# Kernel tuning notes

Measured on AMD Instinct MI355X. Metric: run time of the kernel, lower is better.

The kernel has to match this reference:

```python
import jax, jax.numpy as jnp
import numpy as np

ALPHA = 0.2  # LeakyReLU negative slope
NEG_INF = -9e15


def _gat_layer(Wh, adj, a, concat):
    """One GraphAttentionLayer given pre-projected Wh [B,N,F].
    Algebraic split of the concat attention: e[b,i,j] = lrelu(Wh[i]@a1 + Wh[j]@a2),
    identical math to matmul(cat(Wh_i, Wh_j), a)."""
    F_ = Wh.shape[-1]
    f1 = Wh @ a[:F_, 0]   # [B,N]
    f2 = Wh @ a[F_:, 0]   # [B,N]
    e = jax.nn.leaky_relu(f1[:, :, None] + f2[:, None, :], negative_slope=ALPHA)  # [B,N,N]
    e = jnp.where(adj > 0, e, NEG_INF)
    att = jax.nn.softmax(e, axis=-1)            # dropout omitted (eval mode)
    h_prime = jnp.einsum('bij,bjf->bif', att, Wh)
    return jax.nn.elu(h_prime) if concat else h_prime


def setup_inputs() -> dict:
    key = jax.random.key(0)
    ks = jax.random.split(key, 9)
    B, N, Fin, H, nH, Fout = 4, 2048, 512, 128, 4, 256
    x = jax.random.normal(ks[0], (B, N, Fin), dtype=jnp.float32)
    adj = jax.random.randint(ks[1], (B, N, N), 0, 2, dtype=jnp.int32)
    mask = jnp.ones((B, N), dtype=jnp.float32)
    s = 0.05
    W_heads = jax.random.normal(ks[2], (nH, Fin, H), dtype=jnp.float32) * s
    a_heads = jax.random.normal(ks[3], (nH, 2 * H, 1), dtype=jnp.float32) * s
    W_out = jax.random.normal(ks[4], (nH * H, Fout), dtype=jnp.float32) * s
    a_out = jax.random.normal(ks[5], (2 * Fout, 1), dtype=jnp.float32) * s
    W_pool = jax.random.normal(ks[6], (Fout, Fout), dtype=jnp.float32) * s
    b_pool = jax.random.normal(ks[7], (Fout,), dtype=jnp.float32) * s
    return {"x": x, "adj": adj, "mask": mask, "W_heads": W_heads, "a_heads": a_heads,
            "W_out": W_out, "a_out": a_out, "W_pool": W_pool, "b_pool": b_pool}


def reference(x, adj, mask, W_heads, a_heads, W_out, a_out, W_pool, b_pool):
    # multi-head GAT layer, heads concatenated (dropout = identity in eval)
    heads = [_gat_layer(x @ W_heads[h], adj, a_heads[h], concat=True)
             for h in range(W_heads.shape[0])]
    xcat = jnp.concatenate(heads, axis=-1)                 # [B,N,nH*H]
    x_out = _gat_layer(xcat @ W_out, adj, a_out, concat=False)  # [B,N,Fout]
    x_out = x_out * mask[:, :, None]
    pooled = x_out.sum(axis=1) / (mask.sum(axis=1, keepdims=True) + 1e-10)
    graph_embedding = jax.nn.relu(pooled @ W_pool + b_pool)
    return graph_embedding, x_out
```

## Files before the change

kernel.cpp:

```cpp
#include <hip/hip_runtime.h>

typedef unsigned short u16;
typedef __attribute__((ext_vector_type(8))) short s8v;
typedef __attribute__((ext_vector_type(8))) unsigned short us8;
typedef __attribute__((ext_vector_type(4))) float f4v;

#define L2E 1.4426950408889634f

typedef __attribute__((address_space(1))) void gvoid_t;
typedef __attribute__((address_space(3))) void lvoid_t;

__device__ __forceinline__ u16 f2bf(float f) {
  unsigned u = __builtin_bit_cast(unsigned, f);
  return (u16)((u + 0x7FFFu + ((u >> 16) & 1u)) >> 16);
}
__device__ __forceinline__ float bf2f(u16 h) {
  return __builtin_bit_cast(float, ((unsigned)h) << 16);
}
__device__ __forceinline__ f4v mfma16(s8v a, s8v b, f4v c) {
  return __builtin_amdgcn_mfma_f32_16x16x32_bf16(a, b, c, 0, 0, 0);
}
__device__ __forceinline__ float exp2fast(float x) {
#if __has_builtin(__builtin_amdgcn_exp2f)
  return __builtin_amdgcn_exp2f(x);
#else
  return exp2f(x);
#endif
}
__device__ __forceinline__ void stage16(const u16* g, u16* lds_arr, int slot) {
#if __has_builtin(__builtin_amdgcn_global_load_lds)
  __builtin_amdgcn_global_load_lds((gvoid_t*)(g),
      (lvoid_t*)(lds_arr + (size_t)(slot & ~63) * 8), 16, 0, 0);
#else
  *(us8*)(lds_arr + (size_t)slot * 8) = *(const us8*)g;
#endif
}

__global__ __launch_bounds__(256) void prep_x(const float* __restrict__ x,
                                              u16* __restrict__ xb) {
  int i = (blockIdx.x * 256 + threadIdx.x) * 8;
  float4 v0 = *(const float4*)(x + i);
  float4 v1 = *(const float4*)(x + i + 4);
  us8 o;
  o[0] = f2bf(v0.x); o[1] = f2bf(v0.y); o[2] = f2bf(v0.z); o[3] = f2bf(v0.w);
  o[4] = f2bf(v1.x); o[5] = f2bf(v1.y); o[6] = f2bf(v1.z); o[7] = f2bf(v1.w);
  *(us8*)(xb + i) = o;
}

__global__ __launch_bounds__(256) void prep_wall(const float* __restrict__ W,
                                                 u16* __restrict__ Wt) {
  int idx = blockIdx.x * 256 + threadIdx.x;
  int h = idx >> 16, k = (idx >> 7) & 511, f = idx & 127;
  Wt[(size_t)(h * 128 + f) * 512 + k] = f2bf(W[idx]);
}
__global__ __launch_bounds__(256) void prep_wout(const float* __restrict__ W,
                                                 u16* __restrict__ Wt) {
  int idx = blockIdx.x * 256 + threadIdx.x;
  int k = idx >> 8, c = idx & 255;
  Wt[(size_t)c * 512 + k] = f2bf(W[idx]);
}
__global__ __launch_bounds__(256) void prep_adj(const int* __restrict__ adj,
                                                unsigned* __restrict__ adjw) {
  int chunk = blockIdx.x * 4 + (threadIdx.x >> 6);
  int l = threadIdx.x & 63;
  int v = adj[(size_t)chunk * 64 + l];
  unsigned long long m = __ballot(v != 0);
  if (l == 0) {
    ((uint2*)adjw)[chunk] = make_uint2((unsigned)m, (unsigned)(m >> 32));
  }
}

__global__ __launch_bounds__(256) void gemm_bf16(const u16* __restrict__ A,
                                                 const u16* __restrict__ Bt,
                                                 u16* __restrict__ Ct, int CO) {
  const int K = 512, N = 2048;
  int m0 = blockIdx.x * 128;
  int n0 = blockIdx.y * 128;
  int t = threadIdx.x;
  int w = t >> 6, l = t & 63, lr = l & 15, lq = l >> 4;
  int wr = w >> 1, wc = w & 1;
  __shared__ u16 As[2][128 * 32];
  __shared__ u16 Bs[2][128 * 32];
  f4v zero4 = {0.f, 0.f, 0.f, 0.f};
  f4v acc[4][4];
#pragma unroll
  for (int i = 0; i < 4; ++i)
#pragma unroll
    for (int j = 0; j < 4; ++j) acc[i][j] = zero4;

  auto stage = [&](int buf, int kt) {
    int k0 = kt * 32;
    int row = t >> 2, ch = t & 3;
    stage16(A + (size_t)(m0 + row) * K + k0 + ch * 8, As[buf], t);
    stage16(Bt + (size_t)(n0 + row) * K + k0 + ch * 8, Bs[buf], t);
    int s2 = t + 256;
    row = s2 >> 2; ch = s2 & 3;
    stage16(A + (size_t)(m0 + row) * K + k0 + ch * 8, As[buf], s2);
    stage16(Bt + (size_t)(n0 + row) * K + k0 + ch * 8, Bs[buf], s2);
  };
  stage(0, 0);
  for (int kt = 0; kt < 16; ++kt) {
    __syncthreads();
    if (kt < 15) stage((kt + 1) & 1, kt + 1);
    const u16* as = As[kt & 1];
    const u16* bs = Bs[kt & 1];
    s8v af[4], bfr[4];
#pragma unroll
    for (int rf = 0; rf < 4; ++rf)
      af[rf] = *(const s8v*)&as[(wr * 64 + rf * 16 + lr) * 32 + lq * 8];
#pragma unroll
    for (int nf = 0; nf < 4; ++nf)
      bfr[nf] = *(const s8v*)&bs[(wc * 64 + nf * 16 + lr) * 32 + lq * 8];
#pragma unroll
    for (int rf = 0; rf < 4; ++rf)
#pragma unroll
      for (int nf = 0; nf < 4; ++nf)
        acc[rf][nf] = mfma16(af[rf], bfr[nf], acc[rf][nf]);
  }
  int bidx = m0 >> 11;
  int nr0 = m0 & 2047;
#pragma unroll
  for (int rf = 0; rf < 4; ++rf) {
#pragma unroll
    for (int nf = 0; nf < 4; ++nf) {
      int col = n0 + wc * 64 + nf * 16 + lr;
      int nr = nr0 + wr * 64 + rf * 16 + lq * 4;
      f4v a = acc[rf][nf];
      ushort4 v = make_ushort4(f2bf(a[0]), f2bf(a[1]), f2bf(a[2]), f2bf(a[3]));
      *(ushort4*)&Ct[((size_t)bidx * CO + col) * N + nr] = v;
    }
  }
}

__global__ __launch_bounds__(256) void fkern(const u16* __restrict__ Wht,
                                             const float* __restrict__ a,
                                             float* __restrict__ f1L,
                                             float* __restrict__ f2L, int COLS,
                                             int F) {
  const int N = 2048;
  int h = blockIdx.z, b = blockIdx.y;
  int nl = threadIdx.x & 63, fc = threadIdx.x >> 6;
  int n = blockIdx.x * 64 + nl;
  int F4 = F >> 2;
  const u16* colp = Wht + ((size_t)(b * COLS + h * F + fc * F4)) * N + n;
  const float* ah = a + h * 2 * F + fc * F4;
  float a1 = 0.f, a2 = 0.f;
  for (int c = 0; c < F4; ++c) {
    float v = bf2f(colp[(size_t)c * N]);
    a1 = fmaf(v, ah[c], a1);
    a2 = fmaf(v, ah[F + c], a2);
  }
  __shared__ float r1[4][64], r2[4][64];
  r1[fc][nl] = a1;
  r2[fc][nl] = a2;
  __syncthreads();
  if (fc == 0) {
    float s1 = r1[0][nl] + r1[1][nl] + r1[2][nl] + r1[3][nl];
    float s2 = r2[0][nl] + r2[1][nl] + r2[2][nl] + r2[3][nl];
    f1L[(size_t)(h * 4 + b) * N + n] = s1 * L2E;
    f2L[(size_t)(h * 4 + b) * N + n] = s2 * L2E;
  }
}

__global__ __launch_bounds__(256) void fmax_kern(const float* __restrict__ f2L,
                                                 float* __restrict__ f2m) {
  int row = blockIdx.x;
  const float* p = f2L + (size_t)row * 2048;
  int t = threadIdx.x;
  float v = -__builtin_inff();
  for (int k = 0; k < 8; ++k) v = fmaxf(v, p[t + k * 256]);
#pragma unroll
  for (int d = 1; d < 64; d <<= 1) v = fmaxf(v, __shfl_xor(v, d));
  __shared__ float wm[4];
  if ((t & 63) == 0) wm[t >> 6] = v;
  __syncthreads();
  if (t == 0) f2m[row] = fmaxf(fmaxf(wm[0], wm[1]), fmaxf(wm[2], wm[3]));
}

template <int CT, bool ELU>
__global__ __launch_bounds__(256, 2) void attn_kernel(
    const u16* __restrict__ Wht, const float* __restrict__ f1L,
    const float* __restrict__ f2L, const float* __restrict__ f2max,
    const unsigned* __restrict__ adjw, const float* __restrict__ mask,
    void* __restrict__ outp) {
  const int N = 2048;
  constexpr int NCH = CT / 128;
  constexpr int ROWS = 64;
  constexpr int NT = 2048 / ROWS;
  constexpr int FHD = (CT == 512) ? 1 : 0;
  int kb = blockIdx.x;
  int x = kb & 7, g = kb >> 3;
  int p = x + 8 * (g / NT);
  int it = g % NT;
  int b = p / NCH, ch = p % NCH;
  int i0 = it * ROWS, col0 = ch * 128;
  int fh = FHD ? ch : 0;
  int t = threadIdx.x;
  int w = t >> 6, l = t & 63, lr = l & 15, lq = l >> 4;

  __shared__ u16 Vs[2][128 * 64];
  __shared__ unsigned adjs[ROWS * 65];
  __shared__ float f2s[2048];

  const float* f1p = f1L + (size_t)(fh * 4 + b) * N + i0;
  const float* f2p = f2L + (size_t)(fh * 4 + b) * N;
  float f2m = f2max[fh * 4 + b];
  float f1v = f1p[w * 16 + lr];
  float su = f1v + f2m;
  float M = fmaxf(su, 0.2f * su);
  float c1 = f1v - M;
  float c2 = 0.2f * f1v - M;
  const u16* vbase = Wht + (size_t)(b * CT + col0) * 2048;

  for (int i = t; i < ROWS * 64; i += 256) {
    int row = i >> 6, wd = i & 63;
    adjs[row * 65 + wd] = adjw[(size_t)(b * N + i0 + row) * 64 + wd];
  }
  for (int i = t; i < 2048; i += 256) f2s[i] = f2p[i];

  auto stage = [&](int buf, int kt) {
    int k0 = kt * 64;
#pragma unroll
    for (int j2 = 0; j2 < 4; ++j2) {
      int s = j2 * 256 + t;
      int c = s >> 3, q = s & 7;
      stage16(vbase + (size_t)c * 2048 + k0 + (q ^ (c & 7)) * 8, Vs[buf], s);
    }
  };
  stage(0, 0);

  f4v zero4 = {0.f, 0.f, 0.f, 0.f};
  f4v acc[8];
#pragma unroll
  for (int j = 0; j < 8; ++j) acc[j] = zero4;
  float s_ = 0.f;

  for (int kt = 0; kt < 32; ++kt) {
    __syncthreads();
    if (kt < 31) stage((kt + 1) & 1, kt + 1);
    const u16* vs = Vs[kt & 1];
#pragma unroll
    for (int kk = 0; kk < 2; ++kk) {
      int jt = kt * 2 + kk;
      s8v vf[8];
#pragma unroll
      for (int nf = 0; nf < 8; ++nf) {
        int chn = (kk * 4 + lq) ^ (lr & 7);
        vf[nf] = *(const s8v*)&vs[(nf * 16 + lr) * 64 + chn * 8];
      }
      float4 fa = *(const float4*)&f2s[jt * 32 + lq * 8];
      float4 fb = *(const float4*)&f2s[jt * 32 + lq * 8 + 4];
      float f2c[8] = {fa.x, fa.y, fa.z, fa.w, fb.x, fb.y, fb.z, fb.w};
      unsigned aw = adjs[(w * 16 + lr) * 65 + jt];
      union { s8v v; unsigned u[4]; } pk;
#pragma unroll
      for (int ep = 0; ep < 4; ++ep) {
        float t1 = c1 + f2c[2 * ep];
        float t2 = fmaf(0.2f, f2c[2 * ep], c2);
        float p0 = exp2fast(fmaxf(t1, t2));
        p0 = ((aw >> (lq * 8 + 2 * ep)) & 1u) ? p0 : 0.f;
        s_ += p0;
        float t3 = c1 + f2c[2 * ep + 1];
        float t4 = fmaf(0.2f, f2c[2 * ep + 1], c2);
        float p1 = exp2fast(fmaxf(t3, t4));
        p1 = ((aw >> (lq * 8 + 2 * ep + 1)) & 1u) ? p1 : 0.f;
        s_ += p1;
        asm("v_cvt_pk_bf16_f32 %0, %1, %2"
            : "=v"(pk.u[ep]) : "v"(p0), "v"(p1));
      }
      s8v pa = pk.v;
#pragma unroll
      for (int nf = 0; nf < 8; ++nf)
        acc[nf] = mfma16(pa, vf[nf], acc[nf]);
    }
  }
  s_ += __shfl_xor(s_, 16);
  s_ += __shfl_xor(s_, 32);
  float inv = 1.f / fmaxf(s_, 1e-30f);
  f4v i4;
#pragma unroll
  for (int r = 0; r < 4; ++r) i4[r] = __shfl(inv, lq * 4 + r);
  int rowb = i0 + w * 16 + lq * 4;
#pragma unroll
  for (int nf = 0; nf < 8; ++nf) {
    int col = col0 + nf * 16 + lr;
#pragma unroll
    for (int r = 0; r < 4; ++r) {
      float v = acc[nf][r] * i4[r];
      size_t ob = (size_t)(b * N + rowb + r) * CT + col;
      if constexpr (ELU) {
        v = v > 0.f ? v : exp2fast(v * L2E) - 1.f;
        ((u16*)outp)[ob] = f2bf(v);
      } else {
        ((float*)outp)[ob] = v * mask[b * N + rowb + r];
      }
    }
  }
}

__global__ __launch_bounds__(256) void pool1(const float* __restrict__ xout,
                                             const float* __restrict__ mask,
                                             float* __restrict__ pool,
                                             float* __restrict__ den) {
  int b = blockIdx.x >> 6, s = blockIdx.x & 63;
  int c = threadIdx.x;
  int n0 = s * 32;
  float acc = 0.f;
  for (int r = 0; r < 32; ++r)
    acc += xout[((size_t)(b * 2048 + n0 + r)) * 256 + c];
  atomicAdd(&pool[b * 256 + c], acc);
  if (c == 0) {
    float ms = 0.f;
    for (int r = 0; r < 32; ++r) ms += mask[b * 2048 + n0 + r];
    atomicAdd(&den[b], ms);
  }
}
__global__ __launch_bounds__(256) void pool2(const float* __restrict__ pool,
                                             const float* __restrict__ den,
                                             const float* __restrict__ Wp,
                                             const float* __restrict__ bp,
                                             float* __restrict__ out) {
  int b = blockIdx.x, f = threadIdx.x;
  __shared__ float pv[256];
  float inv = 1.f / (den[b] + 1e-10f);
  pv[f] = pool[b * 256 + f] * inv;
  __syncthreads();
  float acc = bp[f];
  for (int c = 0; c < 256; ++c) acc = fmaf(pv[c], Wp[c * 256 + f], acc);
  out[b * 256 + f] = fmaxf(acc, 0.f);
}

extern "C" void kernel_launch(void* const* d_in, const int* in_sizes, int n_in,
                              void* d_out, int out_size, void* d_ws,
                              size_t ws_size, hipStream_t stream) {
  (void)in_sizes; (void)n_in; (void)out_size; (void)ws_size;
  const float* x = (const float*)d_in[0];
  const int* adj = (const int*)d_in[1];
  const float* mask = (const float*)d_in[2];
  const float* Whds = (const float*)d_in[3];
  const float* ahds = (const float*)d_in[4];
  const float* Wout = (const float*)d_in[5];
  const float* aout = (const float*)d_in[6];
  const float* Wpool = (const float*)d_in[7];
  const float* bpool = (const float*)d_in[8];
  float* out = (float*)d_out;

  char* ws = (char*)d_ws;
  size_t off = 0;
  auto take = [&](size_t n) {
    char* p = ws + off;
    off += (n + 255) & ~(size_t)255;
    return p;
  };
  u16* xb = (u16*)take(8192ull * 512 * 2);
  u16* Wta = (u16*)take(512ull * 512 * 2);
  u16* Wto = (u16*)take(256ull * 512 * 2);
  unsigned* adjw = (unsigned*)take(4ull * 2048 * 64 * 4);
  u16* Wht = (u16*)take(4ull * 512 * 2048 * 2);
  float* f1a = (float*)take(4ull * 4 * 2048 * 4);
  float* f2a = (float*)take(4ull * 4 * 2048 * 4);
  u16* xcat = (u16*)take(8192ull * 512 * 2);
  u16* Wh2t = (u16*)take(4ull * 256 * 2048 * 2);
  float* f1b = (float*)take(4ull * 2048 * 4);
  float* f2b = (float*)take(4ull * 2048 * 4);
  float* f2ma = (float*)take(16 * 4);
  float* f2mb = (float*)take(4 * 4);
  float* pool = (float*)take(1024 * 4);
  float* den = (float*)take(256);

  prep_x<<<2048, 256, 0, stream>>>(x, xb);
  prep_wall<<<1024, 256, 0, stream>>>(Whds, Wta);
  prep_wout<<<512, 256, 0, stream>>>(Wout, Wto);
  prep_adj<<<65536, 256, 0, stream>>>(adj, adjw);
  gemm_bf16<<<dim3(64, 4), 256, 0, stream>>>(xb, Wta, Wht, 512);
  fkern<<<dim3(32, 4, 4), 256, 0, stream>>>(Wht, ahds, f1a, f2a, 512, 128);
  fmax_kern<<<16, 256, 0, stream>>>(f2a, f2ma);
  attn_kernel<512, true><<<512, 256, 0, stream>>>(Wht, f1a, f2a, f2ma,
                                                  adjw, nullptr, xcat);
  gemm_bf16<<<dim3(64, 2), 256, 0, stream>>>(xcat, Wto, Wh2t, 256);
  fkern<<<dim3(32, 4, 1), 256, 0, stream>>>(Wh2t, aout, f1b, f2b, 256, 256);
  fmax_kern<<<4, 256, 0, stream>>>(f2b, f2mb);
  attn_kernel<256, false><<<256, 256, 0, stream>>>(Wh2t, f1b, f2b, f2mb,
                                                   adjw, mask, out + 1024);
  hipMemsetAsync(pool, 0, 4096 + 256, stream);
  pool1<<<256, 256, 0, stream>>>(out + 1024, mask, pool, den);
  pool2<<<4, 256, 0, stream>>>(pool, den, Wpool, bpool, out);
}
```

Baseline: 180.5 us.

## Swizzle GEMM LDS tiles, compute softmax sums via MFMA, split second attention by rows/cols

Applies an XOR swizzle to the GEMM's shared-memory A/B tiles to cut LDS bank conflicts on fragment reads. In the attention kernel, the per-row softmax denominator is now computed with an extra MFMA against a ones vector instead of scalar adds plus shuffles. The attention kernel is also templated on a warp-row count, so the second (256-column) layer uses 32-row tiles with two column-warps and launches 512 blocks instead of 256, raising parallelism. The cost is one extra MFMA per step and more redundant exp work per output column in the second layer.

```diff
diff --git a/kernel.cpp b/kernel.cpp
--- a/kernel.cpp
+++ b/kernel.cpp
@@ -91,14 +91,17 @@
   auto stage = [&](int buf, int kt) {
     int k0 = kt * 32;
     int row = t >> 2, ch = t & 3;
-    stage16(A + (size_t)(m0 + row) * K + k0 + ch * 8, As[buf], t);
-    stage16(Bt + (size_t)(n0 + row) * K + k0 + ch * 8, Bs[buf], t);
+    int q = (ch ^ ((row >> 1) & 3)) * 8;
+    stage16(A + (size_t)(m0 + row) * K + k0 + q, As[buf], t);
+    stage16(Bt + (size_t)(n0 + row) * K + k0 + q, Bs[buf], t);
     int s2 = t + 256;
     row = s2 >> 2; ch = s2 & 3;
-    stage16(A + (size_t)(m0 + row) * K + k0 + ch * 8, As[buf], s2);
-    stage16(Bt + (size_t)(n0 + row) * K + k0 + ch * 8, Bs[buf], s2);
+    q = (ch ^ ((row >> 1) & 3)) * 8;
+    stage16(A + (size_t)(m0 + row) * K + k0 + q, As[buf], s2);
+    stage16(Bt + (size_t)(n0 + row) * K + k0 + q, Bs[buf], s2);
   };
   stage(0, 0);
+  int swz = (lq ^ ((lr >> 1) & 3)) * 8;
   for (int kt = 0; kt < 16; ++kt) {
     __syncthreads();
     if (kt < 15) stage((kt + 1) & 1, kt + 1);
@@ -107,10 +110,10 @@
     s8v af[4], bfr[4];
 #pragma unroll
     for (int rf = 0; rf < 4; ++rf)
-      af[rf] = *(const s8v*)&as[(wr * 64 + rf * 16 + lr) * 32 + lq * 8];
+      af[rf] = *(const s8v*)&as[(wr * 64 + rf * 16 + lr) * 32 + swz];
 #pragma unroll
     for (int nf = 0; nf < 4; ++nf)
-      bfr[nf] = *(const s8v*)&bs[(wc * 64 + nf * 16 + lr) * 32 + lq * 8];
+      bfr[nf] = *(const s8v*)&bs[(wc * 64 + nf * 16 + lr) * 32 + swz];
 #pragma unroll
     for (int rf = 0; rf < 4; ++rf)
 #pragma unroll
@@ -177,15 +180,17 @@
   if (t == 0) f2m[row] = fmaxf(fmaxf(wm[0], wm[1]), fmaxf(wm[2], wm[3]));
 }
 
-template <int CT, bool ELU>
+template <int CT, int WR, bool ELU>
 __global__ __launch_bounds__(256, 2) void attn_kernel(
     const u16* __restrict__ Wht, const float* __restrict__ f1L,
     const float* __restrict__ f2L, const float* __restrict__ f2max,
     const unsigned* __restrict__ adjw, const float* __restrict__ mask,
     void* __restrict__ outp) {
   const int N = 2048;
+  constexpr int WC = 4 / WR;
+  constexpr int NF = 8 / WC;
   constexpr int NCH = CT / 128;
-  constexpr int ROWS = 64;
+  constexpr int ROWS = WR * 16;
   constexpr int NT = 2048 / ROWS;
   constexpr int FHD = (CT == 512) ? 1 : 0;
   int kb = blockIdx.x;
@@ -197,6 +202,7 @@
   int fh = FHD ? ch : 0;
   int t = threadIdx.x;
   int w = t >> 6, l = t & 63, lr = l & 15, lq = l >> 4;
+  int wc = w & (WC - 1), wrs = w / WC;
 
   __shared__ u16 Vs[2][128 * 64];
   __shared__ unsigned adjs[ROWS * 65];
@@ -205,7 +211,7 @@
   const float* f1p = f1L + (size_t)(fh * 4 + b) * N + i0;
   const float* f2p = f2L + (size_t)(fh * 4 + b) * N;
   float f2m = f2max[fh * 4 + b];
-  float f1v = f1p[w * 16 + lr];
+  float f1v = f1p[wrs * 16 + lr];
   float su = f1v + f2m;
   float M = fmaxf(su, 0.2f * su);
   float c1 = f1v - M;
@@ -230,10 +236,12 @@
   stage(0, 0);
 
   f4v zero4 = {0.f, 0.f, 0.f, 0.f};
-  f4v acc[8];
-#pragma unroll
-  for (int j = 0; j < 8; ++j) acc[j] = zero4;
-  float s_ = 0.f;
+  f4v acc[NF], accs = zero4;
+#pragma unroll
+  for (int j = 0; j < NF; ++j) acc[j] = zero4;
+  s8v ones;
+#pragma unroll
+  for (int i = 0; i < 8; ++i) ones[i] = (short)0x3F80;
 
   for (int kt = 0; kt < 32; ++kt) {
     __syncthreads();
@@ -242,16 +250,17 @@
 #pragma unroll
     for (int kk = 0; kk < 2; ++kk) {
       int jt = kt * 2 + kk;
-      s8v vf[8];
-#pragma unroll
-      for (int nf = 0; nf < 8; ++nf) {
+      s8v vf[NF];
+#pragma unroll
+      for (int nf = 0; nf < NF; ++nf) {
+        int c = wc * 64 + nf * 16 + lr;
         int chn = (kk * 4 + lq) ^ (lr & 7);
-        vf[nf] = *(const s8v*)&vs[(nf * 16 + lr) * 64 + chn * 8];
+        vf[nf] = *(const s8v*)&vs[c * 64 + chn * 8];
       }
       float4 fa = *(const float4*)&f2s[jt * 32 + lq * 8];
       float4 fb = *(const float4*)&f2s[jt * 32 + lq * 8 + 4];
       float f2c[8] = {fa.x, fa.y, fa.z, fa.w, fb.x, fb.y, fb.z, fb.w};
-      unsigned aw = adjs[(w * 16 + lr) * 65 + jt];
+      unsigned aw = adjs[(wrs * 16 + lr) * 65 + jt];
       union { s8v v; unsigned u[4]; } pk;
 #pragma unroll
       for (int ep = 0; ep < 4; ++ep) {
@@ -259,31 +268,27 @@
         float t2 = fmaf(0.2f, f2c[2 * ep], c2);
         float p0 = exp2fast(fmaxf(t1, t2));
         p0 = ((aw >> (lq * 8 + 2 * ep)) & 1u) ? p0 : 0.f;
-        s_ += p0;
         float t3 = c1 + f2c[2 * ep + 1];
         float t4 = fmaf(0.2f, f2c[2 * ep + 1], c2);
         float p1 = exp2fast(fmaxf(t3, t4));
         p1 = ((aw >> (lq * 8 + 2 * ep + 1)) & 1u) ? p1 : 0.f;
-        s_ += p1;
         asm("v_cvt_pk_bf16_f32 %0, %1, %2"
             : "=v"(pk.u[ep]) : "v"(p0), "v"(p1));
       }
       s8v pa = pk.v;
-#pragma unroll
-      for (int nf = 0; nf < 8; ++nf)
+      accs = mfma16(pa, ones, accs);
+#pragma unroll
+      for (int nf = 0; nf < NF; ++nf)
         acc[nf] = mfma16(pa, vf[nf], acc[nf]);
     }
   }
-  s_ += __shfl_xor(s_, 16);
-  s_ += __shfl_xor(s_, 32);
-  float inv = 1.f / fmaxf(s_, 1e-30f);
   f4v i4;
 #pragma unroll
-  for (int r = 0; r < 4; ++r) i4[r] = __shfl(inv, lq * 4 + r);
-  int rowb = i0 + w * 16 + lq * 4;
-#pragma unroll
-  for (int nf = 0; nf < 8; ++nf) {
-    int col = col0 + nf * 16 + lr;
+  for (int r = 0; r < 4; ++r) i4[r] = 1.f / fmaxf(accs[r], 1e-30f);
+  int rowb = i0 + wrs * 16 + lq * 4;
+#pragma unroll
+  for (int nf = 0; nf < NF; ++nf) {
+    int col = col0 + wc * 64 + nf * 16 + lr;
 #pragma unroll
     for (int r = 0; r < 4; ++r) {
       float v = acc[nf][r] * i4[r];
@@ -375,13 +380,13 @@
   gemm_bf16<<<dim3(64, 4), 256, 0, stream>>>(xb, Wta, Wht, 512);
   fkern<<<dim3(32, 4, 4), 256, 0, stream>>>(Wht, ahds, f1a, f2a, 512, 128);
   fmax_kern<<<16, 256, 0, stream>>>(f2a, f2ma);
-  attn_kernel<512, true><<<512, 256, 0, stream>>>(Wht, f1a, f2a, f2ma,
-                                                  adjw, nullptr, xcat);
+  attn_kernel<512, 4, true><<<512, 256, 0, stream>>>(Wht, f1a, f2a, f2ma,
+                                                     adjw, nullptr, xcat);
   gemm_bf16<<<dim3(64, 2), 256, 0, stream>>>(xcat, Wto, Wh2t, 256);
   fkern<<<dim3(32, 4, 1), 256, 0, stream>>>(Wh2t, aout, f1b, f2b, 256, 256);
   fmax_kern<<<4, 256, 0, stream>>>(f2b, f2mb);
-  attn_kernel<256, false><<<256, 256, 0, stream>>>(Wh2t, f1b, f2b, f2mb,
-                                                   adjw, mask, out + 1024);
+  attn_kernel<256, 2, false><<<512, 256, 0, stream>>>(Wh2t, f1b, f2b, f2mb,
+                                                      adjw, mask, out + 1024);
   hipMemsetAsync(pool, 0, 4096 + 256, stream);
   pool1<<<256, 256, 0, stream>>>(out + 1024, mask, pool, den);
   pool2<<<4, 256, 0, stream>>>(pool, den, Wpool, bpool, out);
```

Measured after the change: 174.4 us. -3.4%, faster.
